# Kernel tuning notes

Measured on AMD Instinct MI355X. Metric: run time of the kernel, lower is better.

Reference implementation:

```python
import jax, jax.numpy as jnp
import numpy as np

N = 12288
IN_F = 128
OUT_F = 64
ALPHA = 0.2  # LeakyReLU negative slope
NEG_INF = -9e15


def setup_inputs() -> dict:
    key = jax.random.key(0)
    k1, k2, k3, k4 = jax.random.split(key, 4)
    input = jax.random.normal(k1, (N, IN_F), dtype=jnp.float32)
    adj = jax.random.randint(k2, (N, N), 0, 2, dtype=jnp.int32)
    # xavier-uniform-ish init with gain 1.414
    limW = 1.414 * np.sqrt(6.0 / (IN_F + OUT_F))
    W = jax.random.uniform(k3, (IN_F, OUT_F), dtype=jnp.float32, minval=-limW, maxval=limW)
    lima = 1.414 * np.sqrt(6.0 / (2 * OUT_F + 1))
    a = jax.random.uniform(k4, (2 * OUT_F, 1), dtype=jnp.float32, minval=-lima, maxval=lima)
    return {"input": input, "adj": adj, "W": W, "a": a}


def reference(input, adj, W, a):
    # h: (N, out_features)
    h = input @ W
    # broadcast attention logits: e[i,j] = leakyrelu(h_i . a1 + h_j . a2)
    Wh1 = h @ a[:OUT_F, :]          # (N, 1)
    Wh2 = h @ a[OUT_F:, :]          # (N, 1)
    e = Wh1 + Wh2.T                  # (N, N)
    e = jnp.where(e > 0, e, ALPHA * e)  # leaky relu
    # mask by adjacency, row softmax
    attention = jnp.where(adj > 0, e, NEG_INF)
    attention = jax.nn.softmax(attention, axis=1)
    # dropout is identity in eval mode (training=False)
    h_prime = attention @ h          # (N, out_features)
    return jax.nn.elu(h_prime)
```

## Files before the change

kernel.cpp:

```cpp
#include <hip/hip_runtime.h>

#define NN 12288
#define OUTF 64
#define ALPHA 0.2f
#define C1 6.0f

typedef unsigned short u16;
typedef unsigned int u32;
typedef unsigned long long u64;
typedef _Float16 half8 __attribute__((ext_vector_type(8)));
typedef float floatx4 __attribute__((ext_vector_type(4)));
typedef int intx4 __attribute__((ext_vector_type(4)));

union H16 { u16 u; _Float16 h; };
__device__ __forceinline__ u16 f2h(float f) { H16 c; c.h = (_Float16)f; return c.u; }

__global__ __launch_bounds__(256) void k1_prep(
    const float* __restrict__ inp, const float* __restrict__ W, const float* __restrict__ a,
    u16* __restrict__ e1h, u16* __restrict__ thh,
    float* __restrict__ f1g, float* __restrict__ f2g, u16* __restrict__ Btf)
{
  __shared__ float Wl[128 * 64];
  __shared__ float hsm[16][66];
  __shared__ float e1sm[16], e2sm[16];
  const int tid = threadIdx.x;
  for (int t = tid; t < 128 * 64 / 4; t += 256)
    ((float4*)Wl)[t] = ((const float4*)W)[t];
  const int wave = tid >> 6, lane = tid & 63;
  const int k16 = blockIdx.x;
  const float a1l = a[lane], a2l = a[OUTF + lane];
  __syncthreads();
  for (int jl = 0; jl < 4; ++jl) {
    const int jn = wave * 4 + jl;
    const int j = k16 * 16 + jn;
    const float4* xp = (const float4*)(inp + (size_t)j * 128);
    float h = 0.f;
#pragma unroll
    for (int c4 = 0; c4 < 32; ++c4) {
      float4 v = xp[c4];
      const int k = c4 * 4;
      h += v.x * Wl[k * 64 + lane] + v.y * Wl[(k + 1) * 64 + lane]
         + v.z * Wl[(k + 2) * 64 + lane] + v.w * Wl[(k + 3) * 64 + lane];
    }
    float p1 = h * a1l, p2 = h * a2l;
#pragma unroll
    for (int off = 32; off > 0; off >>= 1) { p1 += __shfl_xor(p1, off); p2 += __shfl_xor(p2, off); }
    hsm[jn][lane] = h;
    if (lane == 0) {
      const float s1 = p1, s2 = p2;
      const float e1 = expf(s2 - C1), e2 = expf(ALPHA * s2);
      e1sm[jn] = e1; e2sm[jn] = e2;
      e1h[j] = f2h(e1);
      thh[j] = f2h(expf(-s1 - C1));
      f1g[j] = expf(s1 + C1);
      f2g[j] = expf(ALPHA * s1);
    }
  }
  __syncthreads();
  const int k32 = k16 >> 1, hi = (k16 & 1) * 32;
  for (int cc = tid; cc < 320; cc += 256) {
    const int n = cc >> 5, l32 = cc & 31;
    const int r = n * 16 + (l32 & 15);
    const int jb = (l32 >> 4) * 8;
    u32 wpk[4];
#pragma unroll
    for (int p = 0; p < 4; ++p) {
      u16 hh[2];
#pragma unroll
      for (int q2 = 0; q2 < 2; ++q2) {
        const int jj = jb + p * 2 + q2;
        float v;
        if (r < 64)        v = e1sm[jj] * hsm[jj][r];
        else if (r == 64)  v = e1sm[jj];
        else if (r < 80)   v = 0.f;
        else if (r < 144)  v = e2sm[jj] * hsm[jj][r - 80];
        else if (r == 144) v = e2sm[jj];
        else               v = 0.f;
        hh[q2] = f2h(v);
      }
      wpk[p] = (u32)hh[0] | ((u32)hh[1] << 16);
    }
    ((uint4*)Btf)[(size_t)(k32 * 10 + n) * 64 + hi + l32] = make_uint4(wpk[0], wpk[1], wpk[2], wpk[3]);
  }
}

__global__ __launch_bounds__(256) void k_pack(
    const int* __restrict__ adj, const u16* __restrict__ e1h, const u16* __restrict__ thh,
    unsigned char* __restrict__ P1, unsigned char* __restrict__ P2)
{
  const int i = blockIdx.x, tid = threadIdx.x;
  const u16 th = thh[i];
  const int* arow = adj + (size_t)i * NN;
  unsigned char* p1r = P1 + (size_t)i * (NN / 8);
  unsigned char* p2r = P2 + (size_t)i * (NN / 8);
#pragma unroll
  for (int it = 0; it < NN / 2048; ++it) {
    const int cb = it * 2048 + tid * 8;
    intx4 a0 = *reinterpret_cast<const intx4*>(arow + cb);
    intx4 a1 = *reinterpret_cast<const intx4*>(arow + cb + 4);
    uint4 ev = *reinterpret_cast<const uint4*>(e1h + cb);
    const int av[8] = {a0.x, a0.y, a0.z, a0.w, a1.x, a1.y, a1.z, a1.w};
    const u32 ew[4] = {ev.x, ev.y, ev.z, ev.w};
    u32 b1 = 0, b2 = 0;
#pragma unroll
    for (int e = 0; e < 8; ++e) {
      const u16 eh = (u16)(ew[e >> 1] >> ((e & 1) * 16));
      const bool bit = av[e] != 0;
      const bool up = eh > th;
      b1 |= (u32)(bit && up) << e;
      b2 |= (u32)(bit && !up) << e;
    }
    p1r[it * 256 + tid] = (unsigned char)b1;
    p2r[it * 256 + tid] = (unsigned char)b2;
  }
}

__global__ __launch_bounds__(256, 3) void k2_main(
    const u64* __restrict__ P1, const u64* __restrict__ P2,
    const u16* __restrict__ Btf, float* __restrict__ part)
{
  __shared__ float red[32][132];
  const int tid = threadIdx.x;
  const int wave = tid >> 6, lane = tid & 63;
  const int quad = lane >> 4, lr = lane & 15;
  const int mpos = (int)blockIdx.x >> 1;
  const int khalf = (int)blockIdx.x & 1;
  const int mbase = mpos * 32;

  for (int i = tid; i < 32 * 132; i += 256) (&red[0][0])[i] = 0.f;

  const u64* b1p[2] = {P1 + (size_t)(mbase + lr) * (NN / 64),
                       P1 + (size_t)(mbase + 16 + lr) * (NN / 64)};
  const u64* b2p[2] = {P2 + (size_t)(mbase + lr) * (NN / 64),
                       P2 + (size_t)(mbase + 16 + lr) * (NN / 64)};
  const int k0 = khalf * (NN / 2) + wave * (NN / 8);

  floatx4 acc[2][10];
#pragma unroll
  for (int t = 0; t < 2; ++t)
#pragma unroll
    for (int n = 0; n < 10; ++n) acc[t][n] = (floatx4){0.f, 0.f, 0.f, 0.f};

  __syncthreads();

  for (int kb = k0; kb < k0 + NN / 8; kb += 64) {
    const u64 b1a = b1p[0][kb >> 6], b1b = b1p[1][kb >> 6];
    const u64 b2a = b2p[0][kb >> 6], b2b = b2p[1][kb >> 6];
#pragma unroll
    for (int h = 0; h < 2; ++h) {
      const int k32 = (kb >> 5) + h;
      const u32 sh = (u32)(h * 32 + quad * 8);
      union { half8 v; u16 s[8]; } A1[2], A2[2];
      const u32 m1a = (u32)(b1a >> sh) & 0xFFu, m2a = (u32)(b2a >> sh) & 0xFFu;
      const u32 m1b = (u32)(b1b >> sh) & 0xFFu, m2b = (u32)(b2b >> sh) & 0xFFu;
#pragma unroll
      for (int e = 0; e < 8; ++e) {
        A1[0].s[e] = ((m1a >> e) & 1u) ? (u16)0x3C00 : (u16)0;
        A2[0].s[e] = ((m2a >> e) & 1u) ? (u16)0x3C00 : (u16)0;
        A1[1].s[e] = ((m1b >> e) & 1u) ? (u16)0x3C00 : (u16)0;
        A2[1].s[e] = ((m2b >> e) & 1u) ? (u16)0x3C00 : (u16)0;
      }
      const half8* bp = reinterpret_cast<const half8*>(Btf + ((size_t)k32 * 10 * 64 + lane) * 8);
#pragma unroll
      for (int n = 0; n < 10; ++n) {
        half8 Bv = bp[n * 64];
        acc[0][n] = __builtin_amdgcn_mfma_f32_16x16x32_f16(n < 5 ? A1[0].v : A2[0].v, Bv,
                                                           acc[0][n], 0, 0, 0);
        acc[1][n] = __builtin_amdgcn_mfma_f32_16x16x32_f16(n < 5 ? A1[1].v : A2[1].v, Bv,
                                                           acc[1][n], 0, 0, 0);
      }
    }
  }

#pragma unroll
  for (int t = 0; t < 2; ++t) {
#pragma unroll
    for (int n = 0; n < 4; ++n)
#pragma unroll
      for (int r = 0; r < 4; ++r)
        atomicAdd(&red[t * 16 + quad * 4 + r][n * 16 + lr], acc[t][n][r]);
#pragma unroll
    for (int n = 5; n < 9; ++n)
#pragma unroll
      for (int r = 0; r < 4; ++r)
        atomicAdd(&red[t * 16 + quad * 4 + r][64 + (n - 5) * 16 + lr], acc[t][n][r]);
    if (lr == 0) {
#pragma unroll
      for (int r = 0; r < 4; ++r) {
        atomicAdd(&red[t * 16 + quad * 4 + r][128], acc[t][4][r]);
        atomicAdd(&red[t * 16 + quad * 4 + r][129], acc[t][9][r]);
      }
    }
  }
  __syncthreads();

  float* pp = part + ((size_t)khalf * 384 + mpos) * (32 * 132);
  for (int i = tid; i < 32 * 132; i += 256) pp[i] = (&red[0][0])[i];
}

__global__ __launch_bounds__(256) void k3_final(
    const float* __restrict__ part, const float* __restrict__ f1g,
    const float* __restrict__ f2g, float* __restrict__ out)
{
  const int gid = blockIdx.x * 256 + threadIdx.x;
  const int row = gid >> 6, col = gid & 63;
  const int mpos = row >> 5, r = row & 31;
  const float* pa = part + ((size_t)mpos) * (32 * 132) + r * 132;
  const float* pb = part + ((size_t)(384 + mpos)) * (32 * 132) + r * 132;
  const float n1 = pa[col] + pb[col];
  const float n2 = pa[64 + col] + pb[64 + col];
  const float d1 = pa[128] + pb[128];
  const float d2 = pa[129] + pb[129];
  const float f1 = f1g[row], f2 = f2g[row];
  const float num = f1 * n1 + f2 * n2;
  const float den = fmaxf(f1 * d1 + f2 * d2, 1e-30f);
  const float x = num / den;
  out[gid] = x > 0.f ? x : (expf(x) - 1.f);
}

extern "C" void kernel_launch(void* const* d_in, const int* in_sizes, int n_in,
                              void* d_out, int out_size, void* d_ws, size_t ws_size,
                              hipStream_t stream) {
  const float* inp = (const float*)d_in[0];
  const int* adj = (const int*)d_in[1];
  const float* W = (const float*)d_in[2];
  const float* a = (const float*)d_in[3];

  char* ws = (char*)d_ws;
  u16* Btf = (u16*)ws;
  unsigned char* P1 = (unsigned char*)(ws + 3932160);
  unsigned char* P2 = P1 + 18874368;
  float* part = (float*)(ws + 3932160 + 2 * 18874368);
  char* tail = ws + 3932160 + 2 * 18874368 + 12976128;
  u16* e1h = (u16*)tail;
  u16* thh = e1h + NN;
  float* f1g = (float*)(thh + NN);
  float* f2g = f1g + NN;

  k1_prep<<<768, 256, 0, stream>>>(inp, W, a, e1h, thh, f1g, f2g, Btf);
  k_pack<<<NN, 256, 0, stream>>>(adj, e1h, thh, P1, P2);
  k2_main<<<768, 256, 0, stream>>>((const u64*)P1, (const u64*)P2, Btf, part);
  k3_final<<<NN * OUTF / 256, 256, 0, stream>>>(part, f1g, f2g, (float*)d_out);
}
```

Before: 1.044 ms.

## Share B tiles across waves via double-buffered LDS and split K eight ways

After: 898.8 us. 1.16x faster.

```diff
diff --git a/kernel.cpp b/kernel.cpp
--- a/kernel.cpp
+++ b/kernel.cpp
@@ -4,6 +4,9 @@
 #define OUTF 64
 #define ALPHA 0.2f
 #define C1 6.0f
+#define KSP 8
+#define KRANGE (NN / KSP)
+#define ITERS (KRANGE / 64)
 
 typedef unsigned short u16;
 typedef unsigned int u32;
@@ -119,21 +122,17 @@
     const u64* __restrict__ P1, const u64* __restrict__ P2,
     const u16* __restrict__ Btf, float* __restrict__ part)
 {
-  __shared__ float red[32][132];
+  __shared__ u16 sB[2][10240];
   const int tid = threadIdx.x;
   const int wave = tid >> 6, lane = tid & 63;
   const int quad = lane >> 4, lr = lane & 15;
-  const int mpos = (int)blockIdx.x >> 1;
-  const int khalf = (int)blockIdx.x & 1;
-  const int mbase = mpos * 32;
-
-  for (int i = tid; i < 32 * 132; i += 256) (&red[0][0])[i] = 0.f;
-
-  const u64* b1p[2] = {P1 + (size_t)(mbase + lr) * (NN / 64),
-                       P1 + (size_t)(mbase + 16 + lr) * (NN / 64)};
-  const u64* b2p[2] = {P2 + (size_t)(mbase + lr) * (NN / 64),
-                       P2 + (size_t)(mbase + 16 + lr) * (NN / 64)};
-  const int k0 = khalf * (NN / 2) + wave * (NN / 8);
+  const int mpos = (int)blockIdx.x >> 3;
+  const int ks = (int)blockIdx.x & 7;
+  const int mbase = mpos * 128 + wave * 32;
+  const int k0 = ks * KRANGE;
+
+  const u64* p1r[2] = {P1 + (size_t)(mbase + lr) * 192, P1 + (size_t)(mbase + 16 + lr) * 192};
+  const u64* p2r[2] = {P2 + (size_t)(mbase + lr) * 192, P2 + (size_t)(mbase + 16 + lr) * 192};
 
   floatx4 acc[2][10];
 #pragma unroll
@@ -141,18 +140,45 @@
 #pragma unroll
     for (int n = 0; n < 10; ++n) acc[t][n] = (floatx4){0.f, 0.f, 0.f, 0.f};
 
-  __syncthreads();
-
-  for (int kb = k0; kb < k0 + NN / 8; kb += 64) {
-    const u64 b1a = b1p[0][kb >> 6], b1b = b1p[1][kb >> 6];
-    const u64 b2a = b2p[0][kb >> 6], b2b = b2p[1][kb >> 6];
+  const uint4* gB = (const uint4*)Btf;
+  {
+    const uint4* src = gB + (size_t)(k0 >> 5) * 640;
+#pragma unroll
+    for (int i = 0; i < 5; ++i) ((uint4*)sB[0])[tid + i * 256] = src[tid + i * 256];
+  }
+
+  u64 P1w[2], P2w[2];
+  for (int it = 0; it < ITERS; ++it) {
+    __syncthreads();
+    const int cur = it & 1;
+    uint4 stg[5];
+    const bool more = (it + 1 < ITERS);
+    if (more) {
+      const uint4* src = gB + (size_t)((k0 + (it + 1) * 64) >> 5) * 640;
+#pragma unroll
+      for (int i = 0; i < 5; ++i) stg[i] = src[tid + i * 256];
+    }
+    if ((it & 3) == 0) {
+      const int kw0 = (k0 >> 6) + it;
+#pragma unroll
+      for (int t = 0; t < 2; ++t) {
+        P1w[t] = p1r[t][kw0 + quad];
+        P2w[t] = p2r[t][kw0 + quad];
+      }
+    }
+    const int j = it & 3;
+    u64 b1[2], b2[2];
+#pragma unroll
+    for (int t = 0; t < 2; ++t) {
+      b1[t] = __shfl(P1w[t], (j << 4) | lr);
+      b2[t] = __shfl(P2w[t], (j << 4) | lr);
+    }
 #pragma unroll
     for (int h = 0; h < 2; ++h) {
-      const int k32 = (kb >> 5) + h;
       const u32 sh = (u32)(h * 32 + quad * 8);
       union { half8 v; u16 s[8]; } A1[2], A2[2];
-      const u32 m1a = (u32)(b1a >> sh) & 0xFFu, m2a = (u32)(b2a >> sh) & 0xFFu;
-      const u32 m1b = (u32)(b1b >> sh) & 0xFFu, m2b = (u32)(b2b >> sh) & 0xFFu;
+      const u32 m1a = (u32)(b1[0] >> sh) & 0xFFu, m2a = (u32)(b2[0] >> sh) & 0xFFu;
+      const u32 m1b = (u32)(b1[1] >> sh) & 0xFFu, m2b = (u32)(b2[1] >> sh) & 0xFFu;
 #pragma unroll
       for (int e = 0; e < 8; ++e) {
         A1[0].s[e] = ((m1a >> e) & 1u) ? (u16)0x3C00 : (u16)0;
@@ -160,42 +186,41 @@
         A1[1].s[e] = ((m1b >> e) & 1u) ? (u16)0x3C00 : (u16)0;
         A2[1].s[e] = ((m2b >> e) & 1u) ? (u16)0x3C00 : (u16)0;
       }
-      const half8* bp = reinterpret_cast<const half8*>(Btf + ((size_t)k32 * 10 * 64 + lane) * 8);
+      const u16* bp = &sB[cur][h * 5120];
 #pragma unroll
       for (int n = 0; n < 10; ++n) {
-        half8 Bv = bp[n * 64];
+        half8 Bv = *(const half8*)(bp + (n * 64 + lane) * 8);
         acc[0][n] = __builtin_amdgcn_mfma_f32_16x16x32_f16(n < 5 ? A1[0].v : A2[0].v, Bv,
                                                            acc[0][n], 0, 0, 0);
         acc[1][n] = __builtin_amdgcn_mfma_f32_16x16x32_f16(n < 5 ? A1[1].v : A2[1].v, Bv,
                                                            acc[1][n], 0, 0, 0);
       }
     }
-  }
-
+    if (more) {
+      const int nb = cur ^ 1;
+#pragma unroll
+      for (int i = 0; i < 5; ++i) ((uint4*)sB[nb])[tid + i * 256] = stg[i];
+    }
+  }
+
+  const int ks96 = ks * 96 + mpos;
 #pragma unroll
   for (int t = 0; t < 2; ++t) {
-#pragma unroll
-    for (int n = 0; n < 4; ++n)
-#pragma unroll
-      for (int r = 0; r < 4; ++r)
-        atomicAdd(&red[t * 16 + quad * 4 + r][n * 16 + lr], acc[t][n][r]);
-#pragma unroll
-    for (int n = 5; n < 9; ++n)
-#pragma unroll
-      for (int r = 0; r < 4; ++r)
-        atomicAdd(&red[t * 16 + quad * 4 + r][64 + (n - 5) * 16 + lr], acc[t][n][r]);
-    if (lr == 0) {
-#pragma unroll
-      for (int r = 0; r < 4; ++r) {
-        atomicAdd(&red[t * 16 + quad * 4 + r][128], acc[t][4][r]);
-        atomicAdd(&red[t * 16 + quad * 4 + r][129], acc[t][9][r]);
-      }
-    }
-  }
-  __syncthreads();
-
-  float* pp = part + ((size_t)khalf * 384 + mpos) * (32 * 132);
-  for (int i = tid; i < 32 * 132; i += 256) pp[i] = (&red[0][0])[i];
+    float* pp = part + ((size_t)ks96 * 128 + wave * 32 + t * 16 + quad * 4) * 132;
+#pragma unroll
+    for (int r = 0; r < 4; ++r) {
+#pragma unroll
+      for (int n = 0; n < 4; ++n)
+        pp[r * 132 + n * 16 + lr] = acc[t][n][r];
+#pragma unroll
+      for (int n = 5; n < 9; ++n)
+        pp[r * 132 + 64 + (n - 5) * 16 + lr] = acc[t][n][r];
+      if (lr == 0) {
+        pp[r * 132 + 128] = acc[t][4][r];
+        pp[r * 132 + 129] = acc[t][9][r];
+      }
+    }
+  }
 }
 
 __global__ __launch_bounds__(256) void k3_final(
@@ -204,13 +229,13 @@
 {
   const int gid = blockIdx.x * 256 + threadIdx.x;
   const int row = gid >> 6, col = gid & 63;
-  const int mpos = row >> 5, r = row & 31;
-  const float* pa = part + ((size_t)mpos) * (32 * 132) + r * 132;
-  const float* pb = part + ((size_t)(384 + mpos)) * (32 * 132) + r * 132;
-  const float n1 = pa[col] + pb[col];
-  const float n2 = pa[64 + col] + pb[64 + col];
-  const float d1 = pa[128] + pb[128];
-  const float d2 = pa[129] + pb[129];
+  const int mpos = row >> 7, r = row & 127;
+  float n1 = 0.f, n2 = 0.f, d1 = 0.f, d2 = 0.f;
+#pragma unroll
+  for (int ks = 0; ks < KSP; ++ks) {
+    const float* p = part + ((size_t)(ks * 96 + mpos) * 128 + r) * 132;
+    n1 += p[col]; n2 += p[64 + col]; d1 += p[128]; d2 += p[129];
+  }
   const float f1 = f1g[row], f2 = f2g[row];
   const float num = f1 * n1 + f2 * n2;
   const float den = fmaxf(f1 * d1 + f2 * d2, 1e-30f);
@@ -231,7 +256,7 @@
   unsigned char* P1 = (unsigned char*)(ws + 3932160);
   unsigned char* P2 = P1 + 18874368;
   float* part = (float*)(ws + 3932160 + 2 * 18874368);
-  char* tail = ws + 3932160 + 2 * 18874368 + 12976128;
+  char* tail = ws + 3932160 + 2 * 18874368 + 51904512;
   u16* e1h = (u16*)tail;
   u16* thh = e1h + NN;
   float* f1g = (float*)(thh + NN);
```
